# Kernel tuning notes

Hardware: AMD Instinct MI355X
Metric: run time of the kernel (lower is better)

## Reference

```python
import jax, jax.numpy as jnp
import numpy as np

N, C, F_OUT, H, W, K = 16, 3, 64, 256, 256, 3


def setup_inputs() -> dict:
    key = jax.random.key(0)
    k1, k2, k3 = jax.random.split(key, 3)
    x = jax.random.normal(k1, (N, C, H, W), dtype=jnp.float32)
    # kaiming_uniform-ish init scale (faithful magnitudes, exact dist irrelevant)
    fan_in = C * K * K
    bound_w = jnp.sqrt(6.0 / fan_in)
    weight = jax.random.uniform(k2, (F_OUT, C, K, K), dtype=jnp.float32,
                                minval=-bound_w, maxval=bound_w)
    bound_b = 1.0 / jnp.sqrt(fan_in)
    bias = jax.random.uniform(k3, (F_OUT,), dtype=jnp.float32,
                              minval=-bound_b, maxval=bound_b)
    return {"input": x, "weight": weight, "bias": bias}


def _conv2dcq(x, weight, bias):
    # Faithful to the source: weight3 is overwritten per channel, so only the
    # LAST weight input-channel survives; FHEDot consumes input3[i][0], i.e.
    # only input channel 0's im2col patches. FHEDot is a plain dot product.
    n, c, h, w = x.shape
    f = weight.shape[0]
    w3 = weight[:, c - 1].reshape(f, K * K)          # (F, 9)
    x0 = x[:, 0]                                      # (N, H, W)
    ho, wo = h - K + 1, w - K + 1
    # im2col patches for the 3x3 valid window: (N, Ho, Wo, 9)
    patches = jnp.stack(
        [x0[:, a:a + ho, b:b + wo] for a in range(K) for b in range(K)],
        axis=-1)
    out = jnp.einsum('fk,nhwk->nfhw', w3, patches)    # (N, F, Ho, Wo)
    return out + bias[None, :, None, None]


def reference(input, weight, bias):
    return _conv2dcq(input, weight, bias)
```

## Files before the change

### kernel.cpp

```cpp
#include <hip/hip_runtime.h>

#define NN   16
#define CC   3
#define FOUT 64
#define HH   256
#define WW   256
#define KK   3
#define HO   254
#define WO   254
#define FSPLIT 4
#define FPW  (FOUT / FSPLIT)

typedef float f32x4_a8 __attribute__((ext_vector_type(4), aligned(8)));

__global__ __launch_bounds__(256) void conv2dcq_kernel(
    const float* __restrict__ x,
    const float* __restrict__ weight,
    const float* __restrict__ bias,
    float* __restrict__ out)
{
    __shared__ __align__(16) float w_lds[FOUT][12];

    const int tid = threadIdx.x;
    for (int idx = tid; idx < FOUT * 10; idx += 256) {
        const int f = idx / 10, k = idx - f * 10;
        w_lds[f][k] = (k < 9)
            ? weight[f * (CC * KK * KK) + (CC - 1) * (KK * KK) + k]
            : bias[f];
    }
    __syncthreads();

    const int lane = tid & 63;
    const int wave = tid >> 6;

    const int row = blockIdx.x;
    const int n   = row / HO;
    const int i   = row - n * HO;
    const int fbase = wave * FPW;

    const int j = (lane < 63) ? 4 * lane : 250;

    const float* xp = x + (size_t)n * (CC * HH * WW) + (size_t)i * WW + j;
    float in[3][6];
    #pragma unroll
    for (int r = 0; r < 3; ++r) {
        const f32x4_a8 a = *(const f32x4_a8*)(xp + r * WW);
        const float2   c = *(const float2*)(xp + r * WW + 4);
        in[r][0] = a.x; in[r][1] = a.y; in[r][2] = a.z; in[r][3] = a.w;
        in[r][4] = c.x; in[r][5] = c.y;
    }

    float* op = out + ((size_t)n * FOUT + fbase) * (HO * WO) + (size_t)i * WO + j;

    #pragma unroll 4
    for (int f = fbase; f < fbase + FPW; ++f) {
        const f32x4_a8 w0 = *(const f32x4_a8*)(&w_lds[f][0]);
        const f32x4_a8 w1 = *(const f32x4_a8*)(&w_lds[f][4]);
        const float2   wb = *(const float2*)(&w_lds[f][8]);

        const float wv[9] = { w0.x, w0.y, w0.z, w0.w,
                              w1.x, w1.y, w1.z, w1.w, wb.x };
        float acc[4] = { wb.y, wb.y, wb.y, wb.y };
        #pragma unroll
        for (int a = 0; a < 3; ++a) {
            #pragma unroll
            for (int q = 0; q < 3; ++q) {
                const float wq = wv[a * 3 + q];
                #pragma unroll
                for (int c = 0; c < 4; ++c)
                    acc[c] = fmaf(wq, in[a][q + c], acc[c]);
            }
        }

        f32x4_a8 v; v.x = acc[0]; v.y = acc[1]; v.z = acc[2]; v.w = acc[3];
        __builtin_nontemporal_store(v, (f32x4_a8*)op);
        op += HO * WO;
    }
}

extern "C" void kernel_launch(void* const* d_in, const int* in_sizes, int n_in,
                              void* d_out, int out_size, void* d_ws, size_t ws_size,
                              hipStream_t stream) {
    const float* x      = (const float*)d_in[0];
    const float* weight = (const float*)d_in[1];
    const float* bias   = (const float*)d_in[2];
    float* out          = (float*)d_out;

    const int blocks = NN * HO;
    conv2dcq_kernel<<<blocks, 256, 0, stream>>>(x, weight, bias, out);
}
```

Baseline: 303.8 us.

## Restructure conv so each block computes one (n,f) plane with rolling row window

```diff
diff --git a/kernel.cpp b/kernel.cpp
--- a/kernel.cpp
+++ b/kernel.cpp
@@ -8,10 +8,38 @@
 #define KK   3
 #define HO   254
 #define WO   254
-#define FSPLIT 4
-#define FPW  (FOUT / FSPLIT)
 
-typedef float f32x4_a8 __attribute__((ext_vector_type(4), aligned(8)));
+typedef float f32x4 __attribute__((ext_vector_type(4), aligned(16)));
+
+template <int S0, int S1, int S2, bool ODD>
+__device__ __forceinline__ f32x4 crow(const f32x4* A, const f32x4* B,
+                                      const float* w, float bv)
+{
+    float win[3][6];
+    const int ss[3] = {S0, S1, S2};
+    #pragma unroll
+    for (int r = 0; r < 3; ++r) {
+        const int s = ss[r];
+        if (!ODD) {
+            win[r][0] = A[s][0]; win[r][1] = A[s][1]; win[r][2] = A[s][2];
+            win[r][3] = A[s][3]; win[r][4] = B[s][0]; win[r][5] = B[s][1];
+        } else {
+            win[r][0] = A[s][2]; win[r][1] = A[s][3]; win[r][2] = B[s][0];
+            win[r][3] = B[s][1]; win[r][4] = B[s][2]; win[r][5] = B[s][3];
+        }
+    }
+    f32x4 acc = {bv, bv, bv, bv};
+    #pragma unroll
+    for (int dr = 0; dr < 3; ++dr)
+        #pragma unroll
+        for (int dc = 0; dc < 3; ++dc) {
+            const float wq = w[dr * 3 + dc];
+            #pragma unroll
+            for (int c = 0; c < 4; ++c)
+                acc[c] = fmaf(wq, win[dr][dc + c], acc[c]);
+        }
+    return acc;
+}
 
 __global__ __launch_bounds__(256) void conv2dcq_kernel(
     const float* __restrict__ x,
@@ -19,63 +47,71 @@
     const float* __restrict__ bias,
     float* __restrict__ out)
 {
-    __shared__ __align__(16) float w_lds[FOUT][12];
-
-    const int tid = threadIdx.x;
-    for (int idx = tid; idx < FOUT * 10; idx += 256) {
-        const int f = idx / 10, k = idx - f * 10;
-        w_lds[f][k] = (k < 9)
-            ? weight[f * (CC * KK * KK) + (CC - 1) * (KK * KK) + k]
-            : bias[f];
-    }
-    __syncthreads();
-
+    const int tid  = threadIdx.x;
     const int lane = tid & 63;
     const int wave = tid >> 6;
 
-    const int row = blockIdx.x;
-    const int n   = row / HO;
-    const int i   = row - n * HO;
-    const int fbase = wave * FPW;
+    const int bid = (int)blockIdx.x;
+    const int swz = (bid & 7) * 128 + (bid >> 3);
+    const int n = swz >> 6;
+    const int f = swz & 63;
 
-    const int j = (lane < 63) ? 4 * lane : 250;
+    const int i0   = wave * 64;
+    const int rows = (wave == 3) ? 62 : 64;
 
-    const float* xp = x + (size_t)n * (CC * HH * WW) + (size_t)i * WW + j;
-    float in[3][6];
+    const float* wp = weight + f * (CC * KK * KK) + (CC - 1) * (KK * KK);
+    float w[9];
     #pragma unroll
-    for (int r = 0; r < 3; ++r) {
-        const f32x4_a8 a = *(const f32x4_a8*)(xp + r * WW);
-        const float2   c = *(const float2*)(xp + r * WW + 4);
-        in[r][0] = a.x; in[r][1] = a.y; in[r][2] = a.z; in[r][3] = a.w;
-        in[r][4] = c.x; in[r][5] = c.y;
+    for (int k = 0; k < 9; ++k) w[k] = wp[k];
+    const float bv = bias[f];
+
+    const int colA = (lane < 63) ? 4 * lane     : 252;
+    const int colB = (lane < 63) ? 4 * lane + 4 : 0;
+
+    const float* xrow = x + (size_t)n * (CC * HH * WW);
+    float* op = out + ((size_t)n * FOUT + f) * (HO * WO) + (size_t)i0 * WO;
+
+    f32x4 A[4], B[4];
+
+#define LOADROW(s, r) do {                                             \
+        A[s] = *(const f32x4*)(xrow + (size_t)(r) * WW + colA);        \
+        B[s] = *(const f32x4*)(xrow + (size_t)(r) * WW + colB);        \
+    } while (0)
+
+#define STORE_E(acc) do {                                              \
+        if (lane < 63) *(f32x4*)(op + colA) = (acc);                   \
+        else *(float2*)(op + colA) = make_float2((acc)[0], (acc)[1]);  \
+    } while (0)
+#define STORE_O(acc) do {                                              \
+        if (lane < 63) *(f32x4*)(op + colA + 2) = (acc);               \
+        else *(float2*)(op) = make_float2((acc)[2], (acc)[3]);         \
+    } while (0)
+
+    LOADROW(0, i0 + 0);
+    LOADROW(1, i0 + 1);
+    LOADROW(2, i0 + 2);
+
+    int r = i0;
+    const int nIter = rows >> 2;
+    for (int it = 0; it < nIter; ++it, r += 4) {
+        LOADROW(3, r + 3);
+        { f32x4 a = crow<0,1,2,false>(A, B, w, bv); STORE_E(a); op += WO; }
+        LOADROW(0, r + 4);
+        { f32x4 a = crow<1,2,3,true >(A, B, w, bv); STORE_O(a); op += WO; }
+        LOADROW(1, r + 5);
+        { f32x4 a = crow<2,3,0,false>(A, B, w, bv); STORE_E(a); op += WO; }
+        LOADROW(2, r + 6);
+        { f32x4 a = crow<3,0,1,true >(A, B, w, bv); STORE_O(a); op += WO; }
+    }
+    if (rows & 2) {
+        LOADROW(3, r + 3);
+        { f32x4 a = crow<0,1,2,false>(A, B, w, bv); STORE_E(a); op += WO; }
+        { f32x4 a = crow<1,2,3,true >(A, B, w, bv); STORE_O(a); }
     }
 
-    float* op = out + ((size_t)n * FOUT + fbase) * (HO * WO) + (size_t)i * WO + j;
-
-    #pragma unroll 4
-    for (int f = fbase; f < fbase + FPW; ++f) {
-        const f32x4_a8 w0 = *(const f32x4_a8*)(&w_lds[f][0]);
-        const f32x4_a8 w1 = *(const f32x4_a8*)(&w_lds[f][4]);
-        const float2   wb = *(const float2*)(&w_lds[f][8]);
-
-        const float wv[9] = { w0.x, w0.y, w0.z, w0.w,
-                              w1.x, w1.y, w1.z, w1.w, wb.x };
-        float acc[4] = { wb.y, wb.y, wb.y, wb.y };
-        #pragma unroll
-        for (int a = 0; a < 3; ++a) {
-            #pragma unroll
-            for (int q = 0; q < 3; ++q) {
-                const float wq = wv[a * 3 + q];
-                #pragma unroll
-                for (int c = 0; c < 4; ++c)
-                    acc[c] = fmaf(wq, in[a][q + c], acc[c]);
-            }
-        }
-
-        f32x4_a8 v; v.x = acc[0]; v.y = acc[1]; v.z = acc[2]; v.w = acc[3];
-        __builtin_nontemporal_store(v, (f32x4_a8*)op);
-        op += HO * WO;
-    }
+#undef LOADROW
+#undef STORE_E
+#undef STORE_O
 }
 
 extern "C" void kernel_launch(void* const* d_in, const int* in_sizes, int n_in,
@@ -86,6 +122,6 @@
     const float* bias   = (const float*)d_in[2];
     float* out          = (float*)d_out;
 
-    const int blocks = NN * HO;
+    const int blocks = NN * FOUT;
     conv2dcq_kernel<<<blocks, 256, 0, stream>>>(x, weight, bias, out);
 }
```

Measured after the change: 301.1 us. No clear change (-0.9%).
